# Kernel optimization log

Hardware: AMD Instinct MI355X
Metric: run time of the kernel (lower is better)

The kernel has to match this reference:

```python
import jax, jax.numpy as jnp
import numpy as np

N = 50000
E = 800000
IN_CH = 128
HID = 32
HEADS = 8
OUT_CH = 64
NEG_SLOPE = 0.2


def _gat_layer(x, W, att_src, att_dst, bias, src, dst, H, C, concat):
    """One GATConv layer (add aggregation, self-loops appended).
    x: [n, Fin], W: [Fin, H*C], att_*: [H, C], bias: [H*C] or [C].
    src/dst: [E] int edge endpoints (no self loops; they are appended here).
    """
    n = x.shape[0]
    xs = (x @ W).reshape(n, H, C)                 # projected features [n,H,C]
    a_src = (xs * att_src).sum(-1)                # [n,H]
    a_dst = (xs * att_dst).sum(-1)                # [n,H]
    loop = jnp.arange(n, dtype=src.dtype)
    s = jnp.concatenate([src, loop])              # [E+n]
    d = jnp.concatenate([dst, loop])
    alpha = a_src[s] + a_dst[d]                   # per-edge score [E+n,H]
    alpha = jax.nn.leaky_relu(alpha, NEG_SLOPE)
    # segment softmax over destination node (every node has a self loop,
    # so no empty segments)
    amax = jax.ops.segment_max(alpha, d, num_segments=n)
    ex = jnp.exp(alpha - amax[d])
    denom = jax.ops.segment_sum(ex, d, num_segments=n)
    alpha = ex / denom[d]                         # normalized attention [E+n,H]
    # weighted scatter-add aggregation
    out = jax.ops.segment_sum(alpha[:, :, None] * xs[s], d, num_segments=n)
    out = out.reshape(n, H * C) if concat else out.mean(axis=1)
    return out + bias


def setup_inputs() -> dict:
    key = jax.random.key(0)
    ks = jax.random.split(key, 12)
    def glorot(k, shape):
        fan = shape[0] + shape[-1]
        return jax.random.uniform(k, shape, jnp.float32,
                                  -jnp.sqrt(6.0 / fan), jnp.sqrt(6.0 / fan))
    x = jax.random.normal(ks[0], (N, IN_CH), jnp.float32)
    edge_index = jax.random.randint(ks[1], (2, E), 0, N, dtype=jnp.int64)
    W1 = glorot(ks[2], (IN_CH, HEADS * HID))
    att_src1 = glorot(ks[3], (HEADS, HID))
    att_dst1 = glorot(ks[4], (HEADS, HID))
    bias1 = jnp.zeros((HEADS * HID,), jnp.float32)
    W2 = glorot(ks[5], (HEADS * HID, 1 * OUT_CH))
    att_src2 = glorot(ks[6], (1, OUT_CH))
    att_dst2 = glorot(ks[7], (1, OUT_CH))
    bias2 = jnp.zeros((OUT_CH,), jnp.float32)
    return {"x": x, "edge_index": edge_index,
            "W1": W1, "att_src1": att_src1, "att_dst1": att_dst1, "bias1": bias1,
            "W2": W2, "att_src2": att_src2, "att_dst2": att_dst2, "bias2": bias2}


def reference(x, edge_index, W1, att_src1, att_dst1, bias1,
              W2, att_src2, att_dst2, bias2):
    src, dst = edge_index[0], edge_index[1]
    h = _gat_layer(x, W1, att_src1, att_dst1, bias1, src, dst,
                   HEADS, HID, concat=True)      # [N, HEADS*HID]
    h = jax.nn.elu(h)
    out = _gat_layer(h, W2, att_src2, att_dst2, bias2, src, dst,
                     1, OUT_CH, concat=False)    # [N, OUT_CH]
    return out
```

## Files before the change

### kernel.cpp

```cpp
#include <hip/hip_runtime.h>

#define NN 50000
#define NE 800000
#define IN_CH 128
#define HID 32
#define HEADS 8
#define HC 256
#define OUT_CH 64
#define NEG_SLOPE 0.2f
#define SCAN_BLOCKS 196

typedef _Float16 half4 __attribute__((ext_vector_type(4)));
typedef _Float16 half8 __attribute__((ext_vector_type(8)));
typedef float    f32x4 __attribute__((ext_vector_type(4)));


__global__ void hist_kernel(const int* __restrict__ dst, int* __restrict__ deg) {
    int e = blockIdx.x * blockDim.x + threadIdx.x;
    if (e < NE) atomicAdd(&deg[dst[e]], 1);
}

__global__ __launch_bounds__(256)
void scan_phase1(const int* __restrict__ deg, int* __restrict__ excl,
                 int* __restrict__ bsum) {
    __shared__ int sm[256];
    const int t = blockIdx.x * 256 + threadIdx.x;
    const int v = (t < NN) ? deg[t] : 0;
    sm[threadIdx.x] = v;
    __syncthreads();
    for (int off = 1; off < 256; off <<= 1) {
        int u = (threadIdx.x >= off) ? sm[threadIdx.x - off] : 0;
        __syncthreads();
        sm[threadIdx.x] += u;
        __syncthreads();
    }
    if (t < NN) excl[t] = sm[threadIdx.x] - v;
    if (threadIdx.x == 255) bsum[blockIdx.x] = sm[255];
}

__global__ __launch_bounds__(256)
void scan_phase2(const int* __restrict__ bsum, int* __restrict__ boff,
                 int* __restrict__ offsets) {
    __shared__ int sm[256];
    const int t = threadIdx.x;
    const int v = (t < SCAN_BLOCKS) ? bsum[t] : 0;
    sm[t] = v;
    __syncthreads();
    for (int off = 1; off < 256; off <<= 1) {
        int u = (t >= off) ? sm[t - off] : 0;
        __syncthreads();
        sm[t] += u;
        __syncthreads();
    }
    if (t < SCAN_BLOCKS) boff[t] = sm[t] - v;
    if (t == 255) offsets[NN] = sm[255];
}

__global__ __launch_bounds__(256)
void scan_phase3(const int* __restrict__ excl, const int* __restrict__ boff,
                 int* __restrict__ offsets, int* __restrict__ cursor) {
    const int t = blockIdx.x * 256 + threadIdx.x;
    if (t < NN) {
        int v = excl[t] + boff[blockIdx.x];
        offsets[t] = v;
        cursor[t]  = v;
    }
}

__global__ void scatter_kernel(const int* __restrict__ src,
                               const int* __restrict__ dst,
                               int* __restrict__ cursor, int* __restrict__ ssrc,
                               int* __restrict__ sdst) {
    int e = blockIdx.x * blockDim.x + threadIdx.x;
    if (e < NE) {
        int d = dst[e];
        int pos = atomicAdd(&cursor[d], 1);
        ssrc[pos] = src[e];
        sdst[pos] = d;
    }
}


__global__ void cast_f32_f16(const float* __restrict__ in, _Float16* __restrict__ out,
                             int n8) {
    int i = blockIdx.x * blockDim.x + threadIdx.x;
    if (i >= n8) return;
    float4 a = ((const float4*)in)[i * 2];
    float4 b = ((const float4*)in)[i * 2 + 1];
    half8 h;
    h[0] = (_Float16)a.x; h[1] = (_Float16)a.y; h[2] = (_Float16)a.z; h[3] = (_Float16)a.w;
    h[4] = (_Float16)b.x; h[5] = (_Float16)b.y; h[6] = (_Float16)b.z; h[7] = (_Float16)b.w;
    ((half8*)out)[i] = h;
}

__global__ void transpose_cast(const float* __restrict__ W, _Float16* __restrict__ Wt,
                               int K, int N) {
    int i = blockIdx.x * blockDim.x + threadIdx.x;
    if (i >= K * N) return;
    int k = i / N, n = i - k * N;
    Wt[(size_t)n * K + k] = (_Float16)W[i];
}

__global__ __launch_bounds__(256)
void gemm_mfma_h(const _Float16* __restrict__ A, const _Float16* __restrict__ Bt,
                 _Float16* __restrict__ C, int M, int N, int K) {
    __shared__ _Float16 Asl[64][136];
    __shared__ _Float16 Btl[64][136];
    const int tid  = threadIdx.x;
    const int wave = tid >> 6, lane = tid & 63;
    const int lr = lane & 15, lk = lane >> 4;
    const int bm = blockIdx.x * 64, bn = blockIdx.y * 64;
    const int sr = tid >> 2;
    const int ss = (tid & 3) * 32;

    f32x4 acc[4];
#pragma unroll
    for (int i = 0; i < 4; ++i) acc[i] = (f32x4){0.f, 0.f, 0.f, 0.f};

    for (int k0 = 0; k0 < K; k0 += 128) {
        {
            const int ar = bm + sr;
            half8 v0 = {}, v1 = {}, v2 = {}, v3 = {};
            if (ar < M) {
                const half8* ga = (const half8*)(A + (size_t)ar * K + k0 + ss);
                v0 = ga[0]; v1 = ga[1]; v2 = ga[2]; v3 = ga[3];
            }
            *(half8*)&Asl[sr][ss + 0]  = v0;
            *(half8*)&Asl[sr][ss + 8]  = v1;
            *(half8*)&Asl[sr][ss + 16] = v2;
            *(half8*)&Asl[sr][ss + 24] = v3;
            const half8* gb = (const half8*)(Bt + (size_t)(bn + sr) * K + k0 + ss);
            half8 w0 = gb[0], w1 = gb[1], w2 = gb[2], w3 = gb[3];
            *(half8*)&Btl[sr][ss + 0]  = w0;
            *(half8*)&Btl[sr][ss + 8]  = w1;
            *(half8*)&Btl[sr][ss + 16] = w2;
            *(half8*)&Btl[sr][ss + 24] = w3;
        }
        __syncthreads();
#pragma unroll
        for (int kk = 0; kk < 128; kk += 32) {
            half8 a = *(const half8*)&Asl[wave * 16 + lr][kk + lk * 8];
#pragma unroll
            for (int nt = 0; nt < 4; ++nt) {
                half8 b = *(const half8*)&Btl[nt * 16 + lr][kk + lk * 8];
                acc[nt] = __builtin_amdgcn_mfma_f32_16x16x32_f16(a, b, acc[nt], 0, 0, 0);
            }
        }
        __syncthreads();
    }
#pragma unroll
    for (int nt = 0; nt < 4; ++nt) {
        const int col = bn + nt * 16 + lr;
#pragma unroll
        for (int r = 0; r < 4; ++r) {
            const int m = bm + wave * 16 + lk * 4 + r;
            if (m < M) C[(size_t)m * N + col] = (_Float16)acc[nt][r];
        }
    }
}

__global__ __launch_bounds__(256)
void gemm_mfma_hm(const _Float16* __restrict__ A, const _Float16* __restrict__ Bt,
                  _Float16* __restrict__ C, int M, int N, int K) {
    __shared__ _Float16 Asl[64][136];
    __shared__ _Float16 Btl[64][136];
    const int tid  = threadIdx.x;
    const int wave = tid >> 6, lane = tid & 63;
    const int lr = lane & 15, lk = lane >> 4;
    const int bm = blockIdx.x * 64, bn = blockIdx.y * 64;
    const int sr = tid >> 2;
    const int ss = (tid & 3) * 32;

    f32x4 acc[4];
#pragma unroll
    for (int i = 0; i < 4; ++i) acc[i] = (f32x4){0.f, 0.f, 0.f, 0.f};

    for (int k0 = 0; k0 < K; k0 += 128) {
        {
            const int ar = bm + sr;
            half8 v0 = {}, v1 = {}, v2 = {}, v3 = {};
            if (ar < M) {
                const half8* ga = (const half8*)(A + (size_t)ar * K + k0 + ss);
                v0 = ga[0]; v1 = ga[1]; v2 = ga[2]; v3 = ga[3];
            }
            *(half8*)&Asl[sr][ss + 0]  = v0;
            *(half8*)&Asl[sr][ss + 8]  = v1;
            *(half8*)&Asl[sr][ss + 16] = v2;
            *(half8*)&Asl[sr][ss + 24] = v3;
            const half8* gb = (const half8*)(Bt + (size_t)(bn + sr) * K + k0 + ss);
            half8 w0 = gb[0], w1 = gb[1], w2 = gb[2], w3 = gb[3];
            *(half8*)&Btl[sr][ss + 0]  = w0;
            *(half8*)&Btl[sr][ss + 8]  = w1;
            *(half8*)&Btl[sr][ss + 16] = w2;
            *(half8*)&Btl[sr][ss + 24] = w3;
        }
        __syncthreads();
#pragma unroll
        for (int kk = 0; kk < 128; kk += 32) {
            half8 a = *(const half8*)&Asl[wave * 16 + lr][kk + lk * 8];
#pragma unroll
            for (int nt = 0; nt < 4; ++nt) {
                half8 b = *(const half8*)&Btl[nt * 16 + lr][kk + lk * 8];
                acc[nt] = __builtin_amdgcn_mfma_f32_16x16x32_f16(a, b, acc[nt], 0, 0, 0);
            }
        }
        __syncthreads();
    }
#pragma unroll
    for (int nt = 0; nt < 4; ++nt) {
        const int col = bn + nt * 16 + lr;
        const int hh = col >> 5, cc = col & 31;
#pragma unroll
        for (int r = 0; r < 4; ++r) {
            const int m = bm + wave * 16 + lk * 4 + r;
            if (m < M) C[((size_t)hh * M + m) * 32 + cc] = (_Float16)acc[nt][r];
        }
    }
}


__device__ __forceinline__ float lrelu(float x) { return x > 0.f ? x : NEG_SLOPE * x; }

__global__ void attcoef1(const _Float16* __restrict__ xsh, const float* __restrict__ att_s,
                         const float* __restrict__ att_d,
                         float* __restrict__ asn,
                         float* __restrict__ adn2,
                         float* __restrict__ pself1) {
    int n = blockIdx.x * blockDim.x + threadIdx.x;
    int h = blockIdx.y;
    if (n >= NN) return;
    const _Float16* xp = xsh + ((size_t)h * NN + n) * 32;
    const float* sp = att_s + h * 32;
    const float* dp = att_d + h * 32;
    float as = 0.f, ad = 0.f;
#pragma unroll
    for (int i = 0; i < 4; ++i) {
        half8 v = *(const half8*)(xp + i * 8);
#pragma unroll
        for (int j = 0; j < 8; ++j) {
            float f = (float)v[j];
            as += f * sp[i * 8 + j];
            ad += f * dp[i * 8 + j];
        }
    }
    asn[(size_t)n * 8 + h]  = as;
    adn2[(size_t)n * 8 + h] = ad;
    pself1[(size_t)h * NN + n] = __expf(lrelu(as + ad));
}

__global__ void pedge1(const int* __restrict__ ssrc, const int* __restrict__ sdst,
                       const float* __restrict__ asn, const float* __restrict__ adn2,
                       float* __restrict__ p1) {
    int i = blockIdx.x * blockDim.x + threadIdx.x;
    if (i >= NE) return;
    int s = ssrc[i], d = sdst[i];
    float4 A0 = *(const float4*)(asn + (size_t)s * 8);
    float4 A1 = *(const float4*)(asn + (size_t)s * 8 + 4);
    float4 D0 = *(const float4*)(adn2 + (size_t)d * 8);
    float4 D1 = *(const float4*)(adn2 + (size_t)d * 8 + 4);
    p1[0 * NE + i] = __expf(lrelu(A0.x + D0.x));
    p1[1 * NE + i] = __expf(lrelu(A0.y + D0.y));
    p1[2 * NE + i] = __expf(lrelu(A0.z + D0.z));
    p1[3 * NE + i] = __expf(lrelu(A0.w + D0.w));
    p1[4 * NE + i] = __expf(lrelu(A1.x + D1.x));
    p1[5 * NE + i] = __expf(lrelu(A1.y + D1.y));
    p1[6 * NE + i] = __expf(lrelu(A1.z + D1.z));
    p1[7 * NE + i] = __expf(lrelu(A1.w + D1.w));
}

__global__ void attcoef2(const _Float16* __restrict__ xs, const float* __restrict__ att_s,
                         const float* __restrict__ att_d,
                         float* __restrict__ a_s, float* __restrict__ a_d,
                         float* __restrict__ pself2) {
    int n = blockIdx.x * blockDim.x + threadIdx.x;
    if (n >= NN) return;
    const _Float16* xp = xs + (long)n * 64;
    float as = 0.f, ad = 0.f;
#pragma unroll
    for (int i = 0; i < 8; ++i) {
        half8 v = *(const half8*)(xp + i * 8);
#pragma unroll
        for (int j = 0; j < 8; ++j) {
            float f = (float)v[j];
            as += f * att_s[i * 8 + j];
            ad += f * att_d[i * 8 + j];
        }
    }
    a_s[n] = as;
    a_d[n] = ad;
    pself2[n] = __expf(lrelu(as + ad));
}

__global__ void pedge2(const int* __restrict__ ssrc, const int* __restrict__ sdst,
                       const float* __restrict__ a_s, const float* __restrict__ a_d,
                       float* __restrict__ p2) {
    int i = blockIdx.x * blockDim.x + threadIdx.x;
    if (i >= NE) return;
    p2[i] = __expf(lrelu(a_s[ssrc[i]] + a_d[sdst[i]]));
}


__global__ __launch_bounds__(256)
void agg1(const _Float16* __restrict__ xsh,
          const float* __restrict__ p1,
          const float* __restrict__ pself1,
          const int* __restrict__ offsets, const int* __restrict__ ssrc,
          const float* __restrict__ bias,
          _Float16* __restrict__ out) {
    const int head = blockIdx.x & 7;
    const int grp  = blockIdx.x >> 3;
    const int wave = threadIdx.x >> 6;
    const int lane = threadIdx.x & 63;
    const int slot = lane >> 3;
    const int j4   = (lane & 7) * 4;
    const int n    = grp * 32 + wave * 8 + slot;
    const bool valid = (n < NN);
    const _Float16* xh = xsh + (size_t)head * NN * 32;
    const float* pe = p1 + (size_t)head * NE;

    int beg = 0, end = 0;
    if (valid) { beg = offsets[n]; end = offsets[n + 1]; }
    float den = 0.f, c0 = 0.f, c1 = 0.f, c2 = 0.f, c3 = 0.f;
    int e = beg;
    while (__ballot(e < end) != 0ull) {
        const bool a0 = e < end, a1 = e + 1 < end, a2 = e + 2 < end, a3 = e + 3 < end;
        const int s0 = ssrc[a0 ? e : 0],     s1 = ssrc[a1 ? e + 1 : 0];
        const int s2 = ssrc[a2 ? e + 2 : 0], s3 = ssrc[a3 ? e + 3 : 0];
        const float q0 = a0 ? pe[e] : 0.f,     q1 = a1 ? pe[e + 1] : 0.f;
        const float q2 = a2 ? pe[e + 2] : 0.f, q3 = a3 ? pe[e + 3] : 0.f;
        half4 v0 = *(const half4*)(xh + (size_t)s0 * 32 + j4);
        half4 v1 = *(const half4*)(xh + (size_t)s1 * 32 + j4);
        half4 v2 = *(const half4*)(xh + (size_t)s2 * 32 + j4);
        half4 v3 = *(const half4*)(xh + (size_t)s3 * 32 + j4);
        den += (q0 + q1) + (q2 + q3);
        c0 += q0 * (float)v0[0] + q1 * (float)v1[0] + q2 * (float)v2[0] + q3 * (float)v3[0];
        c1 += q0 * (float)v0[1] + q1 * (float)v1[1] + q2 * (float)v2[1] + q3 * (float)v3[1];
        c2 += q0 * (float)v0[2] + q1 * (float)v1[2] + q2 * (float)v2[2] + q3 * (float)v3[2];
        c3 += q0 * (float)v0[3] + q1 * (float)v1[3] + q2 * (float)v2[3] + q3 * (float)v3[3];
        e += 4;
    }
    if (valid) {
        const float ps = pself1[(size_t)head * NN + n];
        half4 sv = *(const half4*)(xh + (size_t)n * 32 + j4);
        den += ps;
        c0 += ps * (float)sv[0]; c1 += ps * (float)sv[1];
        c2 += ps * (float)sv[2]; c3 += ps * (float)sv[3];
        const float inv = 1.0f / den;
        float4 bb = *(const float4*)(bias + head * 32 + j4);
        float o0 = c0 * inv + bb.x, o1 = c1 * inv + bb.y;
        float o2 = c2 * inv + bb.z, o3 = c3 * inv + bb.w;
        o0 = o0 > 0.f ? o0 : expm1f(o0);
        o1 = o1 > 0.f ? o1 : expm1f(o1);
        o2 = o2 > 0.f ? o2 : expm1f(o2);
        o3 = o3 > 0.f ? o3 : expm1f(o3);
        half4 ho;
        ho[0] = (_Float16)o0; ho[1] = (_Float16)o1;
        ho[2] = (_Float16)o2; ho[3] = (_Float16)o3;
        *(half4*)(out + (size_t)n * HC + head * 32 + j4) = ho;
    }
}

__global__ __launch_bounds__(256)
void agg2(const _Float16* __restrict__ xs,
          const float* __restrict__ p2,
          const float* __restrict__ pself2,
          const int* __restrict__ offsets, const int* __restrict__ ssrc,
          const float* __restrict__ bias,
          float* __restrict__ out) {
    const int grp  = blockIdx.x;
    const int wave = threadIdx.x >> 6;
    const int lane = threadIdx.x & 63;
    const int slot = lane >> 3;
    const int j8   = (lane & 7) * 8;
    const int n    = grp * 32 + wave * 8 + slot;
    const bool valid = (n < NN);

    int beg = 0, end = 0;
    if (valid) { beg = offsets[n]; end = offsets[n + 1]; }
    float den = 0.f;
    float c[8] = {};
    int e = beg;
    while (__ballot(e < end) != 0ull) {
        const bool a0 = e < end, a1 = e + 1 < end;
        const int s0 = ssrc[a0 ? e : 0], s1 = ssrc[a1 ? e + 1 : 0];
        const float q0 = a0 ? p2[e] : 0.f, q1 = a1 ? p2[e + 1] : 0.f;
        half8 v0 = *(const half8*)(xs + (size_t)s0 * OUT_CH + j8);
        half8 v1 = *(const half8*)(xs + (size_t)s1 * OUT_CH + j8);
        den += q0 + q1;
#pragma unroll
        for (int q = 0; q < 8; ++q)
            c[q] += q0 * (float)v0[q] + q1 * (float)v1[q];
        e += 2;
    }
    if (valid) {
        const float ps = pself2[n];
        half8 sv = *(const half8*)(xs + (size_t)n * OUT_CH + j8);
        den += ps;
#pragma unroll
        for (int q = 0; q < 8; ++q) c[q] += ps * (float)sv[q];
        const float inv = 1.0f / den;
        float4 w0, w1;
        w0.x = c[0] * inv + bias[j8 + 0];
        w0.y = c[1] * inv + bias[j8 + 1];
        w0.z = c[2] * inv + bias[j8 + 2];
        w0.w = c[3] * inv + bias[j8 + 3];
        w1.x = c[4] * inv + bias[j8 + 4];
        w1.y = c[5] * inv + bias[j8 + 5];
        w1.z = c[6] * inv + bias[j8 + 6];
        w1.w = c[7] * inv + bias[j8 + 7];
        *(float4*)(out + (size_t)n * OUT_CH + j8)     = w0;
        *(float4*)(out + (size_t)n * OUT_CH + j8 + 4) = w1;
    }
}


extern "C" void kernel_launch(void* const* d_in, const int* in_sizes, int n_in,
                              void* d_out, int out_size, void* d_ws, size_t ws_size,
                              hipStream_t stream) {
    const float* x     = (const float*)d_in[0];
    const int*   ei    = (const int*)d_in[1];
    const float* W1    = (const float*)d_in[2];
    const float* atts1 = (const float*)d_in[3];
    const float* attd1 = (const float*)d_in[4];
    const float* bias1 = (const float*)d_in[5];
    const float* W2    = (const float*)d_in[6];
    const float* atts2 = (const float*)d_in[7];
    const float* attd2 = (const float*)d_in[8];
    const float* bias2 = (const float*)d_in[9];
    float*       out   = (float*)d_out;

    const int* srcp = ei;
    const int* dstp = ei + NE;

    char* ws = (char*)d_ws;
    size_t off = 0;
    auto alloc = [&](size_t bytes) -> void* {
        void* p = ws + off;
        off += (bytes + 255) & ~(size_t)255;
        return p;
    };
    _Float16* xh     = (_Float16*)alloc((size_t)NN * IN_CH * 2);
    _Float16* xsh1   = (_Float16*)alloc((size_t)NN * HC * 2);
    _Float16* h1h    = (_Float16*)alloc((size_t)NN * HC * 2);
    float*    p1     = (float*)alloc((size_t)HEADS * NE * 4);
    _Float16* W1t    = (_Float16*)alloc((size_t)HC * IN_CH * 2);
    _Float16* W2t    = (_Float16*)alloc((size_t)OUT_CH * HC * 2);
    float*    asn    = (float*)alloc((size_t)NN * 8 * 4);
    float*    adn2   = (float*)alloc((size_t)NN * 8 * 4);
    float*    pself1 = (float*)alloc((size_t)HEADS * NN * 4);
    float*    as2    = (float*)alloc((size_t)NN * 4);
    float*    ad2    = (float*)alloc((size_t)NN * 4);
    float*    pself2 = (float*)alloc((size_t)NN * 4);
    float*    p2     = (float*)alloc((size_t)NE * 4);
    int*   deg      = (int*)alloc((size_t)NN * 4);
    int*   offsets  = (int*)alloc((size_t)(NN + 1) * 4);
    int*   cursor   = (int*)alloc((size_t)NN * 4);
    int*   ssrc     = (int*)alloc((size_t)NE * 4);
    int*   sdst     = (int*)alloc((size_t)NE * 4);
    int*   excl     = (int*)alloc((size_t)NN * 4);
    int*   bsum     = (int*)alloc((size_t)SCAN_BLOCKS * 4);
    int*   boff     = (int*)alloc((size_t)SCAN_BLOCKS * 4);
    _Float16* xs2h = xsh1;

    hipMemsetAsync(deg, 0, (size_t)NN * 4, stream);
    hist_kernel<<<(NE + 255) / 256, 256, 0, stream>>>(dstp, deg);
    scan_phase1<<<SCAN_BLOCKS, 256, 0, stream>>>(deg, excl, bsum);
    scan_phase2<<<1, 256, 0, stream>>>(bsum, boff, offsets);
    scan_phase3<<<SCAN_BLOCKS, 256, 0, stream>>>(excl, boff, offsets, cursor);
    scatter_kernel<<<(NE + 255) / 256, 256, 0, stream>>>(srcp, dstp, cursor, ssrc, sdst);

    cast_f32_f16<<<(NN * IN_CH / 8 + 255) / 256, 256, 0, stream>>>(x, xh, NN * IN_CH / 8);
    transpose_cast<<<(IN_CH * HC + 255) / 256, 256, 0, stream>>>(W1, W1t, IN_CH, HC);
    transpose_cast<<<(HC * OUT_CH + 255) / 256, 256, 0, stream>>>(W2, W2t, HC, OUT_CH);

    {
        dim3 grid((NN + 63) / 64, HC / 64);
        gemm_mfma_hm<<<grid, 256, 0, stream>>>(xh, W1t, xsh1, NN, HC, IN_CH);
    }
    {
        dim3 grid((NN + 255) / 256, HEADS);
        attcoef1<<<grid, 256, 0, stream>>>(xsh1, atts1, attd1, asn, adn2, pself1);
    }
    pedge1<<<(NE + 255) / 256, 256, 0, stream>>>(ssrc, sdst, asn, adn2, p1);
    agg1<<<((NN + 31) / 32) * 8, 256, 0, stream>>>(xsh1, p1, pself1, offsets, ssrc, bias1, h1h);

    {
        dim3 grid((NN + 63) / 64, OUT_CH / 64);
        gemm_mfma_h<<<grid, 256, 0, stream>>>(h1h, W2t, xs2h, NN, OUT_CH, HC);
    }
    attcoef2<<<(NN + 255) / 256, 256, 0, stream>>>(xs2h, atts2, attd2, as2, ad2, pself2);
    pedge2<<<(NE + 255) / 256, 256, 0, stream>>>(ssrc, sdst, as2, ad2, p2);
    agg2<<<(NN + 31) / 32, 256, 0, stream>>>(xs2h, p2, pself2, offsets, ssrc, bias2, out);
}
```

Before: 325.8 us.

## Sort nodes by in-degree for balanced aggregation and widen per-lane loads

Adds a counting sort of nodes by in-degree (histogram, scan, scatter) and makes both aggregation kernels process nodes in that order, so nodes sharing a wave have similar edge counts and the ballot-driven loop diverges less. agg1 now uses 4 lanes per node with half8 loads, covering 16 nodes per wave. agg2 unrolls its edge loop by 4 instead of 2. This adds three small kernels and a memset, loses locality of the node-ordered output writes and self-feature reads, and raises register use.

```diff
diff --git a/kernel.cpp b/kernel.cpp
--- a/kernel.cpp
+++ b/kernel.cpp
@@ -9,6 +9,7 @@
 #define OUT_CH 64
 #define NEG_SLOPE 0.2f
 #define SCAN_BLOCKS 196
+#define DBINS 1024
 
 typedef _Float16 half4 __attribute__((ext_vector_type(4)));
 typedef _Float16 half8 __attribute__((ext_vector_type(8)));
@@ -77,6 +78,38 @@
         int pos = atomicAdd(&cursor[d], 1);
         ssrc[pos] = src[e];
         sdst[pos] = d;
+    }
+}
+
+
+__global__ void deg_hist(const int* __restrict__ deg, int* __restrict__ dh) {
+    int n = blockIdx.x * blockDim.x + threadIdx.x;
+    if (n < NN) atomicAdd(&dh[min(deg[n], DBINS - 1)], 1);
+}
+
+__global__ __launch_bounds__(1024)
+void deg_scan(const int* __restrict__ dh, int* __restrict__ dcur) {
+    __shared__ int sm[DBINS];
+    const int t = threadIdx.x;
+    const int v = dh[t];
+    sm[t] = v;
+    __syncthreads();
+    for (int off = 1; off < DBINS; off <<= 1) {
+        int u = (t >= off) ? sm[t - off] : 0;
+        __syncthreads();
+        sm[t] += u;
+        __syncthreads();
+    }
+    dcur[t] = sm[t] - v;
+}
+
+__global__ void deg_scatter(const int* __restrict__ deg, int* __restrict__ dcur,
+                            int* __restrict__ order) {
+    int n = blockIdx.x * blockDim.x + threadIdx.x;
+    if (n < NN) {
+        int b = min(deg[n], DBINS - 1);
+        int pos = atomicAdd(&dcur[b], 1);
+        order[pos] = n;
     }
 }
 
@@ -305,22 +338,25 @@
           const float* __restrict__ p1,
           const float* __restrict__ pself1,
           const int* __restrict__ offsets, const int* __restrict__ ssrc,
+          const int* __restrict__ order,
           const float* __restrict__ bias,
           _Float16* __restrict__ out) {
     const int head = blockIdx.x & 7;
     const int grp  = blockIdx.x >> 3;
     const int wave = threadIdx.x >> 6;
     const int lane = threadIdx.x & 63;
-    const int slot = lane >> 3;
-    const int j4   = (lane & 7) * 4;
-    const int n    = grp * 32 + wave * 8 + slot;
-    const bool valid = (n < NN);
+    const int slot = lane >> 2;
+    const int j8   = (lane & 3) * 8;
+    const int idx  = grp * 64 + wave * 16 + slot;
+    const bool valid = (idx < NN);
+    const int n = valid ? order[idx] : 0;
     const _Float16* xh = xsh + (size_t)head * NN * 32;
     const float* pe = p1 + (size_t)head * NE;
 
     int beg = 0, end = 0;
     if (valid) { beg = offsets[n]; end = offsets[n + 1]; }
-    float den = 0.f, c0 = 0.f, c1 = 0.f, c2 = 0.f, c3 = 0.f;
+    float den = 0.f;
+    float c[8] = {};
     int e = beg;
     while (__ballot(e < end) != 0ull) {
         const bool a0 = e < end, a1 = e + 1 < end, a2 = e + 2 < end, a3 = e + 3 < end;
@@ -328,35 +364,32 @@
         const int s2 = ssrc[a2 ? e + 2 : 0], s3 = ssrc[a3 ? e + 3 : 0];
         const float q0 = a0 ? pe[e] : 0.f,     q1 = a1 ? pe[e + 1] : 0.f;
         const float q2 = a2 ? pe[e + 2] : 0.f, q3 = a3 ? pe[e + 3] : 0.f;
-        half4 v0 = *(const half4*)(xh + (size_t)s0 * 32 + j4);
-        half4 v1 = *(const half4*)(xh + (size_t)s1 * 32 + j4);
-        half4 v2 = *(const half4*)(xh + (size_t)s2 * 32 + j4);
-        half4 v3 = *(const half4*)(xh + (size_t)s3 * 32 + j4);
+        half8 v0 = *(const half8*)(xh + (size_t)s0 * 32 + j8);
+        half8 v1 = *(const half8*)(xh + (size_t)s1 * 32 + j8);
+        half8 v2 = *(const half8*)(xh + (size_t)s2 * 32 + j8);
+        half8 v3 = *(const half8*)(xh + (size_t)s3 * 32 + j8);
         den += (q0 + q1) + (q2 + q3);
-        c0 += q0 * (float)v0[0] + q1 * (float)v1[0] + q2 * (float)v2[0] + q3 * (float)v3[0];
-        c1 += q0 * (float)v0[1] + q1 * (float)v1[1] + q2 * (float)v2[1] + q3 * (float)v3[1];
-        c2 += q0 * (float)v0[2] + q1 * (float)v1[2] + q2 * (float)v2[2] + q3 * (float)v3[2];
-        c3 += q0 * (float)v0[3] + q1 * (float)v1[3] + q2 * (float)v2[3] + q3 * (float)v3[3];
+#pragma unroll
+        for (int q = 0; q < 8; ++q)
+            c[q] += q0 * (float)v0[q] + q1 * (float)v1[q]
+                  + q2 * (float)v2[q] + q3 * (float)v3[q];
         e += 4;
     }
     if (valid) {
         const float ps = pself1[(size_t)head * NN + n];
-        half4 sv = *(const half4*)(xh + (size_t)n * 32 + j4);
+        half8 sv = *(const half8*)(xh + (size_t)n * 32 + j8);
         den += ps;
-        c0 += ps * (float)sv[0]; c1 += ps * (float)sv[1];
-        c2 += ps * (float)sv[2]; c3 += ps * (float)sv[3];
+#pragma unroll
+        for (int q = 0; q < 8; ++q) c[q] += ps * (float)sv[q];
         const float inv = 1.0f / den;
-        float4 bb = *(const float4*)(bias + head * 32 + j4);
-        float o0 = c0 * inv + bb.x, o1 = c1 * inv + bb.y;
-        float o2 = c2 * inv + bb.z, o3 = c3 * inv + bb.w;
-        o0 = o0 > 0.f ? o0 : expm1f(o0);
-        o1 = o1 > 0.f ? o1 : expm1f(o1);
-        o2 = o2 > 0.f ? o2 : expm1f(o2);
-        o3 = o3 > 0.f ? o3 : expm1f(o3);
-        half4 ho;
-        ho[0] = (_Float16)o0; ho[1] = (_Float16)o1;
-        ho[2] = (_Float16)o2; ho[3] = (_Float16)o3;
-        *(half4*)(out + (size_t)n * HC + head * 32 + j4) = ho;
+        half8 ho;
+#pragma unroll
+        for (int q = 0; q < 8; ++q) {
+            float o = c[q] * inv + bias[head * 32 + j8 + q];
+            o = o > 0.f ? o : expm1f(o);
+            ho[q] = (_Float16)o;
+        }
+        *(half8*)(out + (size_t)n * HC + head * 32 + j8) = ho;
     }
 }
 
@@ -365,6 +398,7 @@
           const float* __restrict__ p2,
           const float* __restrict__ pself2,
           const int* __restrict__ offsets, const int* __restrict__ ssrc,
+          const int* __restrict__ order,
           const float* __restrict__ bias,
           float* __restrict__ out) {
     const int grp  = blockIdx.x;
@@ -372,8 +406,9 @@
     const int lane = threadIdx.x & 63;
     const int slot = lane >> 3;
     const int j8   = (lane & 7) * 8;
-    const int n    = grp * 32 + wave * 8 + slot;
-    const bool valid = (n < NN);
+    const int idx  = grp * 32 + wave * 8 + slot;
+    const bool valid = (idx < NN);
+    const int n = valid ? order[idx] : 0;
 
     int beg = 0, end = 0;
     if (valid) { beg = offsets[n]; end = offsets[n + 1]; }
@@ -381,16 +416,21 @@
     float c[8] = {};
     int e = beg;
     while (__ballot(e < end) != 0ull) {
-        const bool a0 = e < end, a1 = e + 1 < end;
-        const int s0 = ssrc[a0 ? e : 0], s1 = ssrc[a1 ? e + 1 : 0];
-        const float q0 = a0 ? p2[e] : 0.f, q1 = a1 ? p2[e + 1] : 0.f;
+        const bool a0 = e < end, a1 = e + 1 < end, a2 = e + 2 < end, a3 = e + 3 < end;
+        const int s0 = ssrc[a0 ? e : 0],     s1 = ssrc[a1 ? e + 1 : 0];
+        const int s2 = ssrc[a2 ? e + 2 : 0], s3 = ssrc[a3 ? e + 3 : 0];
+        const float q0 = a0 ? p2[e] : 0.f,     q1 = a1 ? p2[e + 1] : 0.f;
+        const float q2 = a2 ? p2[e + 2] : 0.f, q3 = a3 ? p2[e + 3] : 0.f;
         half8 v0 = *(const half8*)(xs + (size_t)s0 * OUT_CH + j8);
         half8 v1 = *(const half8*)(xs + (size_t)s1 * OUT_CH + j8);
-        den += q0 + q1;
+        half8 v2 = *(const half8*)(xs + (size_t)s2 * OUT_CH + j8);
+        half8 v3 = *(const half8*)(xs + (size_t)s3 * OUT_CH + j8);
+        den += (q0 + q1) + (q2 + q3);
 #pragma unroll
         for (int q = 0; q < 8; ++q)
-            c[q] += q0 * (float)v0[q] + q1 * (float)v1[q];
-        e += 2;
+            c[q] += q0 * (float)v0[q] + q1 * (float)v1[q]
+                  + q2 * (float)v2[q] + q3 * (float)v3[q];
+        e += 4;
     }
     if (valid) {
         const float ps = pself2[n];
@@ -460,14 +500,21 @@
     int*   excl     = (int*)alloc((size_t)NN * 4);
     int*   bsum     = (int*)alloc((size_t)SCAN_BLOCKS * 4);
     int*   boff     = (int*)alloc((size_t)SCAN_BLOCKS * 4);
+    int*   dh       = (int*)alloc((size_t)DBINS * 4);
+    int*   dcur     = (int*)alloc((size_t)DBINS * 4);
+    int*   order    = (int*)alloc((size_t)NN * 4);
     _Float16* xs2h = xsh1;
 
     hipMemsetAsync(deg, 0, (size_t)NN * 4, stream);
+    hipMemsetAsync(dh, 0, (size_t)DBINS * 4, stream);
     hist_kernel<<<(NE + 255) / 256, 256, 0, stream>>>(dstp, deg);
     scan_phase1<<<SCAN_BLOCKS, 256, 0, stream>>>(deg, excl, bsum);
     scan_phase2<<<1, 256, 0, stream>>>(bsum, boff, offsets);
     scan_phase3<<<SCAN_BLOCKS, 256, 0, stream>>>(excl, boff, offsets, cursor);
     scatter_kernel<<<(NE + 255) / 256, 256, 0, stream>>>(srcp, dstp, cursor, ssrc, sdst);
+    deg_hist<<<SCAN_BLOCKS, 256, 0, stream>>>(deg, dh);
+    deg_scan<<<1, DBINS, 0, stream>>>(dh, dcur);
+    deg_scatter<<<SCAN_BLOCKS, 256, 0, stream>>>(deg, dcur, order);
 
     cast_f32_f16<<<(NN * IN_CH / 8 + 255) / 256, 256, 0, stream>>>(x, xh, NN * IN_CH / 8);
     transpose_cast<<<(IN_CH * HC + 255) / 256, 256, 0, stream>>>(W1, W1t, IN_CH, HC);
@@ -482,7 +529,8 @@
         attcoef1<<<grid, 256, 0, stream>>>(xsh1, atts1, attd1, asn, adn2, pself1);
     }
     pedge1<<<(NE + 255) / 256, 256, 0, stream>>>(ssrc, sdst, asn, adn2, p1);
-    agg1<<<((NN + 31) / 32) * 8, 256, 0, stream>>>(xsh1, p1, pself1, offsets, ssrc, bias1, h1h);
+    agg1<<<((NN + 63) / 64) * 8, 256, 0, stream>>>(xsh1, p1, pself1, offsets, ssrc,
+                                                   order, bias1, h1h);
 
     {
         dim3 grid((NN + 63) / 64, OUT_CH / 64);
@@ -490,5 +538,6 @@
     }
     attcoef2<<<(NN + 255) / 256, 256, 0, stream>>>(xs2h, atts2, attd2, as2, ad2, pself2);
     pedge2<<<(NE + 255) / 256, 256, 0, stream>>>(ssrc, sdst, as2, ad2, p2);
-    agg2<<<(NN + 31) / 32, 256, 0, stream>>>(xs2h, p2, pself2, offsets, ssrc, bias2, out);
-}
+    agg2<<<(NN + 31) / 32, 256, 0, stream>>>(xs2h, p2, pself2, offsets, ssrc,
+                                             order, bias2, out);
+}
```

Measured after the change: 615.5 us. 1.89x slower.
